# Kernel tuning notes

Hardware: AMD Instinct MI355X
Metric: run time of the kernel (lower is better)

Reference implementation:

```python
import jax, jax.numpy as jnp
import numpy as np
from jax import lax

NUM_HEADS = 4
FIN = 4096
FOUT = 4096


def setup_inputs() -> dict:
    key = jax.random.key(0)
    k1, k2, k3, k4, k5 = jax.random.split(key, 5)
    inp = jax.random.normal(k1, (2, 2048, FIN), dtype=jnp.float32)
    # xavier-uniform-like scale for the fc weight
    lim = float(np.sqrt(6.0 / (FIN + FOUT)))
    W = jax.random.uniform(k2, (FOUT, FIN), minval=-lim, maxval=lim, dtype=jnp.float32)
    # per-head 3x3 conv kernels (Conv2d(1, 1, 3, 3) per head, stacked OIHW)
    conv_w = jax.random.normal(k3, (NUM_HEADS, 1, 3, 3), dtype=jnp.float32) * (1.0 / 3.0)
    conv_b = jax.random.normal(k4, (NUM_HEADS,), dtype=jnp.float32) * 0.1
    sk_wt = jax.random.normal(k5, (NUM_HEADS, 1, 1), dtype=jnp.float32)
    return {"inp": inp, "W": W, "conv_w": conv_w, "conv_b": conv_b, "sk_wt": sk_wt}


def _transform_weight(W, conv_w, conv_b, sk_wt):
    # W: [fout, fin] -> [num_heads, fout/num_heads, fin]
    mat = W.reshape(NUM_HEADS, FOUT // NUM_HEADS, FIN)
    # per-head 3x3 conv == grouped conv with feature_group_count = num_heads
    x = mat[None]  # [1, H=num_heads, fout/h, fin]
    y = lax.conv_general_dilated(
        x, conv_w,
        window_strides=(1, 1),
        padding=((1, 1), (1, 1)),
        feature_group_count=NUM_HEADS,
        dimension_numbers=("NCHW", "OIHW", "NCHW"),
    )[0] + conv_b[:, None, None]
    # sigmoid-gated residual: out + sigmoid(sk_wt) * mat
    out = y + jax.nn.sigmoid(sk_wt) * mat
    return out.reshape(FOUT, FIN)


def reference(inp, W, conv_w, conv_b, sk_wt):
    W_i = _transform_weight(W, conv_w, conv_b, sk_wt)
    # F.linear(inp, W_i) with bias=None
    return jnp.einsum("bsf,of->bso", inp, W_i)
```

## Files before the change

### kernel.cpp

```cpp
#include <hip/hip_runtime.h>
#include <hip/hip_bf16.h>

#define FIN 4096
#define FOUT 4096
#define HEADS 4
#define ROWS_PER_HEAD (FOUT / HEADS)
#define M_DIM 4096

typedef __attribute__((ext_vector_type(8))) short bf16x8;
typedef __attribute__((ext_vector_type(4))) float floatx4;

#define CAST_BLOCKS ((M_DIM * FIN) / (256 * 8))
#define TRANS_BLOCKS 2048

__global__ __launch_bounds__(256) void prep(
    const float* __restrict__ x,
    __hip_bfloat16* __restrict__ y,
    const float* __restrict__ W,
    const float* __restrict__ cw,
    const float* __restrict__ cb,
    const float* __restrict__ sk,
    __hip_bfloat16* __restrict__ Wt) {
  if (blockIdx.x < CAST_BLOCKS) {
    int idx = blockIdx.x * 256 + threadIdx.x;
    const float4* xv = (const float4*)x;
    float4 a = xv[idx * 2];
    float4 b = xv[idx * 2 + 1];
    __hip_bfloat16 t[8];
    t[0] = __float2bfloat16(a.x); t[1] = __float2bfloat16(a.y);
    t[2] = __float2bfloat16(a.z); t[3] = __float2bfloat16(a.w);
    t[4] = __float2bfloat16(b.x); t[5] = __float2bfloat16(b.y);
    t[6] = __float2bfloat16(b.z); t[7] = __float2bfloat16(b.w);
    *(bf16x8*)(&y[(size_t)idx * 8]) = *(bf16x8*)t;
    return;
  }

  int tg = blockIdx.x - CAST_BLOCKS;
  tg = (tg & 7) * (TRANS_BLOCKS / 8) + (tg >> 3);
  const int o0 = (tg >> 1) * 4;
  const int fs = (tg & 1) * 2048 + threadIdx.x * 8;
  const int h = o0 >> 10;
  const int r0 = o0 & (ROWS_PER_HEAD - 1);

  float kk[3][3];
#pragma unroll
  for (int i = 0; i < 3; i++)
#pragma unroll
    for (int j = 0; j < 3; j++) kk[i][j] = cw[h * 9 + i * 3 + j];
  float sig = 1.0f / (1.0f + __expf(-sk[h]));
  float bias = cb[h];

  float w[6][10];
#pragma unroll
  for (int i = 0; i < 6; i++) {
    int rr = r0 - 1 + i;
    if (rr < 0 || rr >= ROWS_PER_HEAD) {
#pragma unroll
      for (int c = 0; c < 10; c++) w[i][c] = 0.0f;
    } else {
      const float* rp = W + ((size_t)(h * ROWS_PER_HEAD + rr)) * FIN + fs;
      float4 v0 = *(const float4*)rp;
      float4 v1 = *(const float4*)(rp + 4);
      w[i][1] = v0.x; w[i][2] = v0.y; w[i][3] = v0.z; w[i][4] = v0.w;
      w[i][5] = v1.x; w[i][6] = v1.y; w[i][7] = v1.z; w[i][8] = v1.w;
      w[i][0] = (fs > 0) ? rp[-1] : 0.0f;
      w[i][9] = (fs + 8 < FIN) ? rp[8] : 0.0f;
    }
  }

#pragma unroll
  for (int j = 0; j < 4; j++) {
    float acc[8];
#pragma unroll
    for (int c = 0; c < 8; c++) acc[c] = bias + sig * w[j + 1][c + 1];
#pragma unroll
    for (int dr = 0; dr < 3; dr++) {
#pragma unroll
      for (int c = 0; c < 8; c++)
        acc[c] += kk[dr][0] * w[j + dr][c] + kk[dr][1] * w[j + dr][c + 1] +
                  kk[dr][2] * w[j + dr][c + 2];
    }
    __hip_bfloat16 t[8];
#pragma unroll
    for (int c = 0; c < 8; c++) t[c] = __float2bfloat16(acc[c]);
    *(bf16x8*)(&Wt[(size_t)(o0 + j) * FIN + fs]) = *(bf16x8*)t;
  }
}

__device__ static inline void gload_lds16(const void* g, void* l) {
  __builtin_amdgcn_global_load_lds(
      (const __attribute__((address_space(1))) void*)g,
      (__attribute__((address_space(3))) void*)l, 16, 0, 0);
}

#define BK 64
#define NT (FIN / BK)

__global__ __launch_bounds__(512, 2) void gemm_nt(
    const __hip_bfloat16* __restrict__ A,
    const __hip_bfloat16* __restrict__ B,
    float* __restrict__ C,
    int M, int N, int K) {
  __shared__ __hip_bfloat16 As0h0[128 * BK];
  __shared__ __hip_bfloat16 As0h1[128 * BK];
  __shared__ __hip_bfloat16 As1h0[128 * BK];
  __shared__ __hip_bfloat16 As1h1[128 * BK];
  __shared__ __hip_bfloat16 Bs0h0[128 * BK];
  __shared__ __hip_bfloat16 Bs0h1[128 * BK];
  __shared__ __hip_bfloat16 Bs1h0[128 * BK];
  __shared__ __hip_bfloat16 Bs1h1[128 * BK];

  const int tid = threadIdx.x;
  const int lane = tid & 63;
  const int wave = tid >> 6;
  const int wr = wave >> 2;
  const int wn = wave & 3;
  const int fr = lane & 15;
  const int quad = lane >> 4;
  const int sel = fr & 7;

  const int orig = blockIdx.y * gridDim.x + blockIdx.x;
  const int swz = (orig & 7) * 32 + (orig >> 3);
  const int tile_m = (swz >> 4) * 256;
  const int tile_n = (swz & 15) * 256;

  const __hip_bfloat16* At = A + (size_t)tile_m * K;
  const __hip_bfloat16* Bt = B + (size_t)tile_n * K;

  int soff[2], doff[2];
#pragma unroll
  for (int c = 0; c < 2; c++) {
    int p = c * 512 + tid;
    int row = p >> 3;
    int g = (p & 7) ^ (row & 7);
    soff[c] = row * K + g * 8;
    doff[c] = p * 8;
  }
  int aro[4], bro[2], co[2];
#pragma unroll
  for (int u = 0; u < 4; u++) aro[u] = (wr * 16 + u * 32 + fr) * 64;
#pragma unroll
  for (int j = 0; j < 2; j++) bro[j] = (wn * 16 + j * 64 + fr) * 64;
#pragma unroll
  for (int kk = 0; kk < 2; kk++) co[kk] = ((kk * 4 + quad) ^ sel) * 8;

  floatx4 acc[8][4];
#pragma unroll
  for (int i = 0; i < 8; i++)
#pragma unroll
    for (int j = 0; j < 4; j++) acc[i][j] = (floatx4){0.f, 0.f, 0.f, 0.f};

  bf16x8 afr[2][4];
  bf16x8 bfr[2][2][2];

#define STAGE(GBASE, DST, TILE, HALF)                                    \
  do {                                                                   \
    const __hip_bfloat16* _s =                                           \
        GBASE + (size_t)(HALF) * 128 * K + (size_t)(TILE) * BK;          \
    _Pragma("unroll") for (int _c = 0; _c < 2; _c++) {                   \
      gload_lds16(_s + soff[_c], DST + doff[_c]);                        \
    }                                                                    \
  } while (0)

#define LOADA4(MS, SRC, KK)                                              \
  do {                                                                   \
    _Pragma("unroll") for (int _u = 0; _u < 4; _u++) {                   \
      afr[MS][_u] = *(const bf16x8*)&SRC[aro[_u] + co[KK]];              \
    }                                                                    \
  } while (0)

#define LOADB2(KS, NH, SRC, KK)                                          \
  do {                                                                   \
    _Pragma("unroll") for (int _j = 0; _j < 2; _j++) {                   \
      bfr[KS][NH][_j] = *(const bf16x8*)&SRC[bro[_j] + co[KK]];          \
    }                                                                    \
  } while (0)

#define MMA8(MS, KS, NH)                                                 \
  do {                                                                   \
    __builtin_amdgcn_s_setprio(1);                                       \
    _Pragma("unroll") for (int _u = 0; _u < 4; _u++) {                   \
      _Pragma("unroll") for (int _j = 0; _j < 2; _j++) {                 \
        acc[(MS) * 4 + _u][(NH) * 2 + _j] =                              \
            __builtin_amdgcn_mfma_f32_16x16x32_bf16(                     \
                afr[MS][_u], bfr[KS][NH][_j],                            \
                acc[(MS) * 4 + _u][(NH) * 2 + _j], 0, 0, 0);             \
      }                                                                  \
    }                                                                    \
    __builtin_amdgcn_s_setprio(0);                                       \
  } while (0)

#define BAR() __builtin_amdgcn_s_barrier()
#define VMC(N) asm volatile("s_waitcnt vmcnt(" #N ")" ::: "memory")
#define FENCE_LGKM(N)                                                    \
  do {                                                                   \
    __builtin_amdgcn_sched_barrier(0);                                   \
    asm volatile("s_waitcnt lgkmcnt(" #N ")" ::: "memory");              \
    __builtin_amdgcn_sched_barrier(0);                                   \
  } while (0)

#define TBODY(T, CA0, CA1, CB0, CB1, NA1, DO_C8, DO_TOP, DO_MID, EVM)    \
  do {                                                                   \
    if (DO_TOP) STAGE(At, NA1, (T) + 1, 1);                              \
    LOADA4(0, CA0, 0);                                          \
    LOADB2(0, 0, CB0, 0);                                                \
    LOADB2(0, 1, CB1, 0);                                                \
    if (DO_C8) MMA8(1, 1, 0);                        \
    FENCE_LGKM(0);                                                       \
    MMA8(0, 0, 0);                                               \
    LOADA4(1, CA1, 0);                                          \
    MMA8(0, 0, 1);                                               \
    LOADB2(1, 0, CB0, 1);                                       \
    LOADB2(1, 1, CB1, 1);                                                \
    LOADA4(0, CA0, 1);                                          \
    FENCE_LGKM(8);                                                       \
    MMA8(1, 0, 1);                                               \
    MMA8(1, 0, 0);                                               \
    LOADA4(1, CA1, 1);                                          \
    FENCE_LGKM(4);                                                       \
    BAR();      \
    if (DO_MID) {                                                        \
      STAGE(At, CA0, (T) + 2, 0);                                        \
      STAGE(Bt, CB0, (T) + 2, 0);                                        \
      STAGE(Bt, CB1, (T) + 2, 1);                                        \
    }                                                                    \
    MMA8(0, 1, 0);                                               \
    MMA8(0, 1, 1);                                               \
    FENCE_LGKM(0);                                                       \
    MMA8(1, 1, 1);                                               \
    if ((EVM) == 2) VMC(6);                                              \
    else if ((EVM) == 1) VMC(0);                                         \
    BAR();                                                               \
  } while (0)

  STAGE(At, As0h0, 0, 0);
  STAGE(Bt, Bs0h0, 0, 0);
  STAGE(Bt, Bs0h1, 0, 1);
  STAGE(At, As0h1, 0, 1);
  STAGE(Bt, Bs1h0, 1, 0);
  STAGE(Bt, Bs1h1, 1, 1);
  STAGE(At, As1h0, 1, 0);
  VMC(6);
  BAR();

  TBODY(0, As0h0, As0h1, Bs0h0, Bs0h1, As1h1, 0, 1, 1, 2);

#pragma unroll 1
  for (int t = 1; t < NT - 3; t += 2) {
    TBODY(t, As1h0, As1h1, Bs1h0, Bs1h1, As0h1, 1, 1, 1, 2);
    TBODY(t + 1, As0h0, As0h1, Bs0h0, Bs0h1, As1h1, 1, 1, 1, 2);
  }

  TBODY(NT - 3, As1h0, As1h1, Bs1h0, Bs1h1, As0h1, 1, 1, 1, 2);
  TBODY(NT - 2, As0h0, As0h1, Bs0h0, Bs0h1, As1h1, 1, 1, 0, 1);
  TBODY(NT - 1, As1h0, As1h1, Bs1h0, Bs1h1, As0h1, 1, 0, 0, 0);
  MMA8(1, 1, 0);

#undef TBODY
#undef FENCE_LGKM
#undef STAGE
#undef LOADA4
#undef LOADB2
#undef MMA8
#undef BAR
#undef VMC

#pragma unroll
  for (int i = 0; i < 8; i++) {
    int mb = tile_m + wr * 16 + i * 32 + quad * 4;
#pragma unroll
    for (int j = 0; j < 4; j++) {
      int n = tile_n + wn * 16 + j * 64 + fr;
#pragma unroll
      for (int r = 0; r < 4; r++) {
        C[(size_t)(mb + r) * N + n] = acc[i][j][r];
      }
    }
  }
}

extern "C" void kernel_launch(void* const* d_in, const int* in_sizes, int n_in,
                              void* d_out, int out_size, void* d_ws,
                              size_t ws_size, hipStream_t stream) {
  const float* inp = (const float*)d_in[0];
  const float* W = (const float*)d_in[1];
  const float* conv_w = (const float*)d_in[2];
  const float* conv_b = (const float*)d_in[3];
  const float* sk_wt = (const float*)d_in[4];
  float* out = (float*)d_out;

  __hip_bfloat16* Wt = (__hip_bfloat16*)d_ws;
  __hip_bfloat16* Ab =
      (__hip_bfloat16*)((char*)d_ws + (size_t)(32u << 20));

  prep<<<CAST_BLOCKS + TRANS_BLOCKS, 256, 0, stream>>>(inp, Ab, W, conv_w,
                                                       conv_b, sk_wt, Wt);
  dim3 grid(FOUT / 256, M_DIM / 256);
  gemm_nt<<<grid, 512, 0, stream>>>(Ab, Wt, out, M_DIM, FOUT, FIN);
}
```

Measured before the change: 288.6 us.

## Load B fragments directly from global into registers, drop B LDS staging

B tiles are no longer staged through shared memory. Each wave now reads its own B MFMA fragments straight from global memory into registers, prefetched one K-step ahead, and only A goes through the LDS double buffer. This halves LDS footprint and LDS read traffic and removes the B staging copies, which could raise occupancy. In exchange, global loads become per-lane 16-byte reads across rows, and each B row is fetched redundantly by the two wave-rows, so the kernel leans more on L2/L1 bandwidth and latency hiding. The wait and barrier schedule is also reworked, which risks stalls or ordering errors.

```diff
diff --git a/kernel.cpp b/kernel.cpp
--- a/kernel.cpp
+++ b/kernel.cpp
@@ -105,10 +105,6 @@
   __shared__ __hip_bfloat16 As0h1[128 * BK];
   __shared__ __hip_bfloat16 As1h0[128 * BK];
   __shared__ __hip_bfloat16 As1h1[128 * BK];
-  __shared__ __hip_bfloat16 Bs0h0[128 * BK];
-  __shared__ __hip_bfloat16 Bs0h1[128 * BK];
-  __shared__ __hip_bfloat16 Bs1h0[128 * BK];
-  __shared__ __hip_bfloat16 Bs1h1[128 * BK];
 
   const int tid = threadIdx.x;
   const int lane = tid & 63;
@@ -125,7 +121,8 @@
   const int tile_n = (swz & 15) * 256;
 
   const __hip_bfloat16* At = A + (size_t)tile_m * K;
-  const __hip_bfloat16* Bt = B + (size_t)tile_n * K;
+  const __hip_bfloat16* Bw =
+      B + (size_t)(tile_n + wn * 16 + fr) * K + quad * 8;
 
   int soff[2], doff[2];
 #pragma unroll
@@ -136,11 +133,9 @@
     soff[c] = row * K + g * 8;
     doff[c] = p * 8;
   }
-  int aro[4], bro[2], co[2];
+  int aro[4], co[2];
 #pragma unroll
   for (int u = 0; u < 4; u++) aro[u] = (wr * 16 + u * 32 + fr) * 64;
-#pragma unroll
-  for (int j = 0; j < 2; j++) bro[j] = (wn * 16 + j * 64 + fr) * 64;
 #pragma unroll
   for (int kk = 0; kk < 2; kk++) co[kk] = ((kk * 4 + quad) ^ sel) * 8;
 
@@ -169,11 +164,14 @@
     }                                                                    \
   } while (0)
 
-#define LOADB2(KS, NH, SRC, KK)                                          \
-  do {                                                                   \
-    _Pragma("unroll") for (int _j = 0; _j < 2; _j++) {                   \
-      bfr[KS][NH][_j] = *(const bf16x8*)&SRC[bro[_j] + co[KK]];          \
-    }                                                                    \
+#define GLB(KS, NH, J, T)                                                \
+  bfr[KS][NH][J] = *(const bf16x8*)(Bw +                                 \
+      (size_t)((NH) * 128 + (J) * 64) * K + (size_t)(T) * 64 + (KS) * 32)
+
+#define GLB4(KS, T)                                                      \
+  do {                                                                   \
+    GLB(KS, 0, 0, T); GLB(KS, 0, 1, T);                                  \
+    GLB(KS, 1, 0, T); GLB(KS, 1, 1, T);                                  \
   } while (0)
 
 #define MMA8(MS, KS, NH)                                                 \
@@ -191,7 +189,7 @@
   } while (0)
 
 #define BAR() __builtin_amdgcn_s_barrier()
-#define VMC(N) asm volatile("s_waitcnt vmcnt(" #N ")" ::: "memory")
+#define WAITVM(N) asm volatile("s_waitcnt vmcnt(" #N ")" ::: "memory")
 #define FENCE_LGKM(N)                                                    \
   do {                                                                   \
     __builtin_amdgcn_sched_barrier(0);                                   \
@@ -199,71 +197,62 @@
     __builtin_amdgcn_sched_barrier(0);                                   \
   } while (0)
 
-#define TBODY(T, CA0, CA1, CB0, CB1, NA1, DO_C8, DO_TOP, DO_MID, EVM)    \
-  do {                                                                   \
-    if (DO_TOP) STAGE(At, NA1, (T) + 1, 1);                              \
+#define TBODY(T, CA0, CA1, NA0, NA1, DO_C8, DO_STAGE, DO_PREF)           \
+  do {                                                                   \
     LOADA4(0, CA0, 0);                                          \
-    LOADB2(0, 0, CB0, 0);                                                \
-    LOADB2(0, 1, CB1, 0);                                                \
-    if (DO_C8) MMA8(1, 1, 0);                        \
+    if (DO_C8) MMA8(1, 1, 0);    \
+    GLB4(1, T);                       \
     FENCE_LGKM(0);                                                       \
     MMA8(0, 0, 0);                                               \
     LOADA4(1, CA1, 0);                                          \
     MMA8(0, 0, 1);                                               \
-    LOADB2(1, 0, CB0, 1);                                       \
-    LOADB2(1, 1, CB1, 1);                                                \
     LOADA4(0, CA0, 1);                                          \
-    FENCE_LGKM(8);                                                       \
+    if (DO_STAGE) {                                                      \
+      STAGE(At, NA0, (T) + 1, 0);                                        \
+      STAGE(At, NA1, (T) + 1, 1);                                        \
+    }                                                                    \
+    FENCE_LGKM(4);                                                       \
     MMA8(1, 0, 1);                                               \
     MMA8(1, 0, 0);                                               \
+    if (DO_PREF) GLB4(0, (T) + 1);    \
     LOADA4(1, CA1, 1);                                          \
     FENCE_LGKM(4);                                                       \
-    BAR();      \
-    if (DO_MID) {                                                        \
-      STAGE(At, CA0, (T) + 2, 0);                                        \
-      STAGE(Bt, CB0, (T) + 2, 0);                                        \
-      STAGE(Bt, CB1, (T) + 2, 1);                                        \
-    }                                                                    \
     MMA8(0, 1, 0);                                               \
     MMA8(0, 1, 1);                                               \
     FENCE_LGKM(0);                                                       \
     MMA8(1, 1, 1);                                               \
-    if ((EVM) == 2) VMC(6);                                              \
-    else if ((EVM) == 1) VMC(0);                                         \
+    if (DO_STAGE) WAITVM(4);                                             \
     BAR();                                                               \
   } while (0)
 
   STAGE(At, As0h0, 0, 0);
-  STAGE(Bt, Bs0h0, 0, 0);
-  STAGE(Bt, Bs0h1, 0, 1);
   STAGE(At, As0h1, 0, 1);
-  STAGE(Bt, Bs1h0, 1, 0);
-  STAGE(Bt, Bs1h1, 1, 1);
-  STAGE(At, As1h0, 1, 0);
-  VMC(6);
+  GLB4(0, 0);
+  WAITVM(4);
   BAR();
 
-  TBODY(0, As0h0, As0h1, Bs0h0, Bs0h1, As1h1, 0, 1, 1, 2);
+  TBODY(0, As0h0, As0h1, As1h0, As1h1, 0, 1, 1);
 
 #pragma unroll 1
   for (int t = 1; t < NT - 3; t += 2) {
-    TBODY(t, As1h0, As1h1, Bs1h0, Bs1h1, As0h1, 1, 1, 1, 2);
-    TBODY(t + 1, As0h0, As0h1, Bs0h0, Bs0h1, As1h1, 1, 1, 1, 2);
-  }
-
-  TBODY(NT - 3, As1h0, As1h1, Bs1h0, Bs1h1, As0h1, 1, 1, 1, 2);
-  TBODY(NT - 2, As0h0, As0h1, Bs0h0, Bs0h1, As1h1, 1, 1, 0, 1);
-  TBODY(NT - 1, As1h0, As1h1, Bs1h0, Bs1h1, As0h1, 1, 0, 0, 0);
+    TBODY(t, As1h0, As1h1, As0h0, As0h1, 1, 1, 1);
+    TBODY(t + 1, As0h0, As0h1, As1h0, As1h1, 1, 1, 1);
+  }
+
+  TBODY(NT - 3, As1h0, As1h1, As0h0, As0h1, 1, 1, 1);
+  TBODY(NT - 2, As0h0, As0h1, As1h0, As1h1, 1, 1, 1);
+  TBODY(NT - 1, As1h0, As1h1, As0h0, As0h1, 1, 0, 0);
   MMA8(1, 1, 0);
 
 #undef TBODY
 #undef FENCE_LGKM
 #undef STAGE
 #undef LOADA4
-#undef LOADB2
+#undef GLB
+#undef GLB4
 #undef MMA8
 #undef BAR
-#undef VMC
+#undef WAITVM
 
 #pragma unroll
   for (int i = 0; i < 8; i++) {
```

Measured after the change: 337.3 us. 1.17x slower.
